# Kernel optimization log

Measured on AMD Instinct MI355X. Metric: run time of the kernel, lower is better.

Reference implementation:

```python
import jax, jax.numpy as jnp
import numpy as np

IMG = 64
N = IMG * IMG          # 4096, spatial tokens = LayerNorm dim
F2 = 128 * 128         # 16384, feature_size**2 = Mlp input dim
B, C = 8, 512
EPS = 1e-5
LOG_MAX = float(np.log(1.0 / 0.01))  # clamp max for logit_scale


def setup_inputs() -> dict:
    key = jax.random.key(0)
    ks = jax.random.split(key, 8)
    s1 = 1.0 / np.sqrt(F2)
    s2 = 1.0 / np.sqrt(N)
    return {
        "x": jax.random.normal(ks[0], (B, C, N), jnp.float32),
        "feature": jax.random.normal(ks[1], (B, C, F2), jnp.float32),
        "fc1_w": jax.random.uniform(ks[2], (N, F2), jnp.float32, -s1, s1),
        "fc1_b": jax.random.uniform(ks[3], (N,), jnp.float32, -s1, s1),
        "fc2_w": jax.random.uniform(ks[4], (N, N), jnp.float32, -s2, s2),
        "fc2_b": jax.random.uniform(ks[5], (N,), jnp.float32, -s2, s2),
        "logit_scale": jnp.full((1, 1, N), np.log(10.0), jnp.float32),
        "norm_w": jnp.ones((N,), jnp.float32),
        "norm_b": jnp.zeros((N,), jnp.float32),
    }


def reference(x, feature, fc1_w, fc1_b, fc2_w, fc2_b, logit_scale, norm_w, norm_b):
    # Mlp: (B,C,F2) -> (B,C,N), ReLU activation, drop=0
    h = jax.nn.relu(jnp.einsum('bcf,nf->bcn', feature, fc1_w) + fc1_b)
    feat = jnp.einsum('bch,nh->bcn', h, fc2_w) + fc2_b        # (B,C,N)
    feat = jnp.swapaxes(feat, 1, 2)                            # (B,N,C)
    scale = jnp.exp(jnp.minimum(logit_scale, LOG_MAX))         # (1,1,N)
    temp = jnp.einsum('bnc,bcm->bnm', feat, x) * scale         # (B,N,N)
    temp = jax.nn.softmax(temp, axis=1)                        # softmax over dim=1
    out = jnp.einsum('bcn,bnm->bcm', x, temp)                  # (B,C,N)
    # LayerNorm over last dim
    mu = jnp.mean(out, axis=-1, keepdims=True)
    var = jnp.var(out, axis=-1, keepdims=True)
    out = (out - mu) * jax.lax.rsqrt(var + EPS) * norm_w + norm_b
    return out
```

## Files before the change

### kernel.cpp

```cpp
#include <hip/hip_runtime.h>
#include <stdint.h>

using u16 = unsigned short;
typedef unsigned int u32;
typedef __attribute__((ext_vector_type(4))) float f32x4;
typedef __attribute__((ext_vector_type(8))) short short8;

typedef const __attribute__((address_space(1))) u32* gas_ptr;
typedef __attribute__((address_space(3))) u32* las_ptr;

__device__ __forceinline__ u16 f2bf_u(float f) {
    u32 u = __builtin_bit_cast(u32, f);
    u32 r = 0x7fffu + ((u >> 16) & 1u);
    return (u16)((u + r) >> 16);
}
__device__ __forceinline__ float bfu2f(u16 h) {
    u32 u = ((u32)h) << 16;
    return __builtin_bit_cast(float, u);
}
__device__ __forceinline__ void split2(float v, u16& hi, u16& lo) {
    hi = f2bf_u(v);
    lo = f2bf_u(v - bfu2f(hi));
}

__device__ __forceinline__ void gload16(const void* g, void* l) {
    __builtin_amdgcn_global_load_lds((gas_ptr)g, (las_ptr)l, 16, 0, 0);
}


#define STAGE(CBUF, KT)                                                      \
  {                                                                          \
    const int kk_ = (KT) << 5;                                               \
    _Pragma("unroll")                                                        \
    for (int it_ = 0; it_ < 2; ++it_) {                                      \
      const int rb_ = it_ * 128 + w * 16;                                    \
      const int lo_ = (CBUF) * 8192 + rb_ * 32;                              \
      const size_t ga_ = (size_t)(brow + rb_ + srow) * lda + (kk_ + sca);    \
      const size_t gb_ = (size_t)(bcol + rb_ + srow) * lda + (kk_ + sca);    \
      gload16(A0 + ga_, &As0[lo_]);                                          \
      gload16(B0 + gb_, &Bs0[lo_]);                                          \
      if constexpr (SPLIT) gload16(A1 + ga_, &As1[lo_]);                     \
    }                                                                        \
  }

#define BLOQ(Q, KT)                                                          \
  {                                                                          \
    const u16* bb_ = B1 + (size_t)(bcol + wc * 64 + lr) * lda                \
                     + (((KT) << 5) + ((l >> 4) * 8));                       \
    _Pragma("unroll")                                                        \
    for (int n_ = 0; n_ < 4; ++n_)                                           \
      Q[n_] = *(const short8*)(bb_ + (size_t)(n_ * 16) * lda);               \
  }

#define PHASE(KT, CBUF, Q)                                                   \
  {                                                                          \
    if ((KT) == NT - 1) {                                                    \
      asm volatile("s_waitcnt vmcnt(0)" ::: "memory");                       \
    } else {                                                                 \
      if constexpr (SPLIT) asm volatile("s_waitcnt vmcnt(10)" ::: "memory"); \
      else asm volatile("s_waitcnt vmcnt(4)" ::: "memory");                  \
    }                                                                        \
    __builtin_amdgcn_s_barrier();                                            \
    __builtin_amdgcn_sched_barrier(0);                                       \
    {                                                                        \
      int cs_ = (CBUF) + 2; if (cs_ >= 3) cs_ -= 3;                          \
      if ((KT) + 2 < NT) STAGE(cs_, (KT) + 2);                               \
    }                                                                        \
    short8 bh_[4];                                                           \
    _Pragma("unroll")                                                        \
    for (int n_ = 0; n_ < 4; ++n_)                                           \
      bh_[n_] = *(const short8*)&Bs0[(CBUF) * 8192 +                         \
                                     (wc * 64 + n_ * 16 + lr) * 32 + cr];    \
    _Pragma("unroll")                                                        \
    for (int mh_ = 0; mh_ < 2; ++mh_) {                                      \
      short8 ah_[4], al_[4];                                                 \
      _Pragma("unroll")                                                      \
      for (int m_ = 0; m_ < 4; ++m_) {                                       \
        const int ro_ = (CBUF) * 8192 +                                      \
                        (wr * 128 + mh_ * 64 + m_ * 16 + lr) * 32 + cr;      \
        ah_[m_] = *(const short8*)&As0[ro_];                                 \
        if constexpr (SPLIT) al_[m_] = *(const short8*)&As1[ro_];            \
      }                                                                      \
      __builtin_amdgcn_s_setprio(1);                                         \
      _Pragma("unroll")                                                      \
      for (int m_ = 0; m_ < 4; ++m_)                                         \
        _Pragma("unroll")                                                    \
        for (int n_ = 0; n_ < 4; ++n_)                                       \
          acc[mh_ * 4 + m_][n_] = __builtin_amdgcn_mfma_f32_16x16x32_bf16(   \
              ah_[m_], bh_[n_], acc[mh_ * 4 + m_][n_], 0, 0, 0);             \
      if constexpr (SPLIT) {                                                 \
        _Pragma("unroll")                                                    \
        for (int m_ = 0; m_ < 4; ++m_)                                       \
          _Pragma("unroll")                                                  \
          for (int n_ = 0; n_ < 4; ++n_)                                     \
            acc[mh_ * 4 + m_][n_] = __builtin_amdgcn_mfma_f32_16x16x32_bf16( \
                al_[m_], bh_[n_], acc[mh_ * 4 + m_][n_], 0, 0, 0);           \
        _Pragma("unroll")                                                    \
        for (int m_ = 0; m_ < 4; ++m_)                                       \
          _Pragma("unroll")                                                  \
          for (int n_ = 0; n_ < 4; ++n_)                                     \
            acc[mh_ * 4 + m_][n_] = __builtin_amdgcn_mfma_f32_16x16x32_bf16( \
                ah_[m_], Q[n_], acc[mh_ * 4 + m_][n_], 0, 0, 0);             \
      }                                                                      \
      __builtin_amdgcn_s_setprio(0);                                         \
    }                                                                        \
    __builtin_amdgcn_sched_barrier(0);                                       \
    if ((KT) + 2 < NT) {                                                     \
      if constexpr (SPLIT) BLOQ(Q, (KT) + 2);                                \
    }                                                                        \
    __builtin_amdgcn_sched_barrier(0);                                       \
  }

template<int EPI, bool SPLIT>
__global__ __launch_bounds__(512, 2)
void gemm256(const u16* __restrict__ Ah, const u16* __restrict__ Al,
             const u16* __restrict__ Bh, const u16* __restrict__ Bl,
             int K, int lda, int N,
             const float* __restrict__ aux,
             void* __restrict__ out0, void* __restrict__ out1,
             size_t strideA, size_t strideB, size_t strideO)
{
    extern __shared__ __align__(16) u16 lds[];
    u16* const As0 = lds;
    u16* const Bs0 = lds + 3 * 8192;
    u16* const As1 = SPLIT ? (lds + 6 * 8192) : lds;

    const int t = threadIdx.x;
    const int w = t >> 6;
    const int l = t & 63;

    int brow, bcol;
    const int gx = gridDim.x, gy = gridDim.y;
    const int orig = blockIdx.y * gx + blockIdx.x;
    if (gx == 16 && gy == 16) {
        const int x = orig & 7, j = orig >> 3;
        brow = ((x & 3) * 4 + (j & 3)) * 256;
        bcol = ((x >> 2) * 8 + (j >> 2)) * 256;
    } else {
        const int nwg = gx * gy;
        const int swz = (orig & 7) * (nwg >> 3) + (orig >> 3);
        brow = (swz / gx) * 256;
        bcol = (swz % gx) * 256;
    }
    const int z = blockIdx.z;

    const u16* A0 = Ah + (size_t)z * strideA;
    const u16* A1 = SPLIT ? (Al + (size_t)z * strideA) : nullptr;
    const u16* B0 = Bh + (size_t)z * strideB;
    const u16* B1 = SPLIT ? (Bl + (size_t)z * strideB) : nullptr;

    const int srow = l >> 2;
    const int sca = ((l & 3) ^ ((l >> 3) & 3)) * 8;

    const int wr = w >> 2;
    const int wc = w & 3;
    const int lr = l & 15;
    const int cr = ((l >> 4) ^ ((l >> 1) & 3)) * 8;

    f32x4 acc[8][4];
    const f32x4 zero = {0.f, 0.f, 0.f, 0.f};
#pragma unroll
    for (int i = 0; i < 8; ++i)
#pragma unroll
        for (int j = 0; j < 4; ++j) acc[i][j] = zero;

    const int NT = K >> 5;
    short8 qA[4], qB[4];

    STAGE(0, 0);
    if constexpr (SPLIT) BLOQ(qA, 0);
    STAGE(1, 1);
    if constexpr (SPLIT) BLOQ(qB, 1);

    int c = 0;
    for (int kt = 0; kt < NT; kt += 2) {
        PHASE(kt, c, qA);
        c = (c == 2) ? 0 : c + 1;
        PHASE(kt + 1, c, qB);
        c = (c == 2) ? 0 : c + 1;
    }

#pragma unroll
    for (int mh = 0; mh < 2; ++mh)
#pragma unroll
        for (int m = 0; m < 4; ++m)
#pragma unroll
            for (int n = 0; n < 4; ++n)
#pragma unroll
                for (int j = 0; j < 4; ++j) {
                    const int row = brow + wr * 128 + mh * 64 + m * 16 + (l >> 4) * 4 + j;
                    const int col = bcol + wc * 64 + n * 16 + (l & 15);
                    float v = acc[mh * 4 + m][n][j];
                    if (EPI == 0) {
                        v += aux[col];
                        v = fmaxf(v, 0.f);
                        u16 hi, lo; split2(v, hi, lo);
                        ((u16*)out0)[(size_t)row * N + col] = hi;
                        ((u16*)out1)[(size_t)row * N + col] = lo;
                    } else if (EPI == 1) {
                        v += aux[col];
                        const int bb = row >> 9, cc = row & 511;
                        const size_t idx = ((size_t)bb * N + col) * 512 + cc;
                        u16 hi, lo; split2(v, hi, lo);
                        ((u16*)out0)[idx] = hi;
                        ((u16*)out1)[idx] = lo;
                    } else if (EPI == 2) {
                        ((float*)out0)[(size_t)row * N + col] = v;
                    } else {
                        ((float*)out0)[(size_t)z * strideO + (size_t)row * N + col] = v;
                    }
                }
}

__global__ void split_k(const float* __restrict__ in, u16* __restrict__ hi,
                        u16* __restrict__ lo, size_t n4)
{
    size_t i = blockIdx.x * (size_t)blockDim.x + threadIdx.x;
    const size_t stride = (size_t)gridDim.x * blockDim.x;
    for (; i < n4; i += stride) {
        const float4 v = ((const float4*)in)[i];
        ushort4 h, l;
        split2(v.x, h.x, l.x);
        split2(v.y, h.y, l.y);
        split2(v.z, h.z, l.z);
        split2(v.w, h.w, l.w);
        ((ushort4*)hi)[i] = h;
        ((ushort4*)lo)[i] = l;
    }
}

__global__ void conv_bf16_k(const float* __restrict__ in, u16* __restrict__ out, size_t n4)
{
    size_t i = blockIdx.x * (size_t)blockDim.x + threadIdx.x;
    const size_t stride = (size_t)gridDim.x * blockDim.x;
    for (; i < n4; i += stride) {
        const float4 v = ((const float4*)in)[i];
        ushort4 o;
        o.x = f2bf_u(v.x); o.y = f2bf_u(v.y); o.z = f2bf_u(v.z); o.w = f2bf_u(v.w);
        ((ushort4*)out)[i] = o;
    }
}

__global__ void transpose_split_x(const float* __restrict__ x,
                                  u16* __restrict__ xt_hi, u16* __restrict__ xt_lo)
{
    __shared__ float tile[32][33];
    const int b = blockIdx.z;
    const int n0 = blockIdx.x * 32;
    const int c0 = blockIdx.y * 32;
    const int tx = threadIdx.x, ty = threadIdx.y;
#pragma unroll
    for (int k = 0; k < 4; ++k)
        tile[ty + 8 * k][tx] = x[((size_t)b * 512 + c0 + ty + 8 * k) * 4096 + n0 + tx];
    __syncthreads();
#pragma unroll
    for (int k = 0; k < 4; ++k) {
        const float v = tile[tx][ty + 8 * k];
        u16 hi, lo; split2(v, hi, lo);
        const size_t idx = ((size_t)b * 4096 + n0 + ty + 8 * k) * 512 + c0 + tx;
        xt_hi[idx] = hi;
        xt_lo[idx] = lo;
    }
}

__global__ void scale_prep(const float* __restrict__ ls, float* __restrict__ s)
{
    const int i = blockIdx.x * blockDim.x + threadIdx.x;
    if (i < 4096) s[i] = expf(fminf(ls[i], 4.605170185988092f));
}

__global__ __launch_bounds__(256)
void softmax_rows(const float* __restrict__ T, const float* __restrict__ s, u16* __restrict__ P)
{
    const int m = blockIdx.x;
    const int t = threadIdx.x;
    const float sc = s[m];
    const float* row = T + (size_t)m * 4096;
    float v[16];
    float mx = -3.402823e38f;
#pragma unroll
    for (int i = 0; i < 16; ++i) {
        v[i] = row[t + 256 * i] * sc;
        mx = fmaxf(mx, v[i]);
    }
#pragma unroll
    for (int o = 32; o; o >>= 1) mx = fmaxf(mx, __shfl_xor(mx, o, 64));
    __shared__ float sm[4], ss[4];
    if ((t & 63) == 0) sm[t >> 6] = mx;
    __syncthreads();
    mx = fmaxf(fmaxf(sm[0], sm[1]), fmaxf(sm[2], sm[3]));
    float sum = 0.f;
#pragma unroll
    for (int i = 0; i < 16; ++i) {
        v[i] = expf(v[i] - mx);
        sum += v[i];
    }
#pragma unroll
    for (int o = 32; o; o >>= 1) sum += __shfl_xor(sum, o, 64);
    if ((t & 63) == 0) ss[t >> 6] = sum;
    __syncthreads();
    sum = (ss[0] + ss[1]) + (ss[2] + ss[3]);
    const float inv = 1.f / sum;
#pragma unroll
    for (int i = 0; i < 16; ++i)
        P[(size_t)m * 4096 + t + 256 * i] = f2bf_u(v[i] * inv);
}

__global__ __launch_bounds__(256)
void ln_rows(const float* __restrict__ X, const float* __restrict__ gw,
             const float* __restrict__ gb, float* __restrict__ out)
{
    const int r = blockIdx.x;
    const int t = threadIdx.x;
    const float* row = X + (size_t)r * 4096;
    float v[16];
    float s1 = 0.f, s2 = 0.f;
#pragma unroll
    for (int i = 0; i < 16; ++i) {
        v[i] = row[t + 256 * i];
        s1 += v[i];
        s2 += v[i] * v[i];
    }
#pragma unroll
    for (int o = 32; o; o >>= 1) {
        s1 += __shfl_xor(s1, o, 64);
        s2 += __shfl_xor(s2, o, 64);
    }
    __shared__ float m1[4], m2[4];
    if ((t & 63) == 0) { m1[t >> 6] = s1; m2[t >> 6] = s2; }
    __syncthreads();
    s1 = (m1[0] + m1[1]) + (m1[2] + m1[3]);
    s2 = (m2[0] + m2[1]) + (m2[2] + m2[3]);
    const float mu = s1 * (1.f / 4096.f);
    const float var = s2 * (1.f / 4096.f) - mu * mu;
    const float rs = rsqrtf(var + 1e-5f);
#pragma unroll
    for (int i = 0; i < 16; ++i) {
        const int n = t + 256 * i;
        out[(size_t)r * 4096 + n] = (v[i] - mu) * rs * gw[n] + gb[n];
    }
}

extern "C" void kernel_launch(void* const* d_in, const int* in_sizes, int n_in,
                              void* d_out, int out_size, void* d_ws, size_t ws_size,
                              hipStream_t stream)
{
    const float* x  = (const float*)d_in[0];
    const float* fe = (const float*)d_in[1];
    const float* w1 = (const float*)d_in[2];
    const float* b1 = (const float*)d_in[3];
    const float* w2 = (const float*)d_in[4];
    const float* b2 = (const float*)d_in[5];
    const float* ls = (const float*)d_in[6];
    const float* nw = (const float*)d_in[7];
    const float* nb = (const float*)d_in[8];
    float* out = (float*)d_out;
    char* ws = (char*)d_ws;

    if (ws_size < 637550592ull) return;

    hipFuncSetAttribute((const void*)gemm256<0, true>,
                        hipFuncAttributeMaxDynamicSharedMemorySize, 147456);
    hipFuncSetAttribute((const void*)gemm256<1, true>,
                        hipFuncAttributeMaxDynamicSharedMemorySize, 147456);
    hipFuncSetAttribute((const void*)gemm256<2, true>,
                        hipFuncAttributeMaxDynamicSharedMemorySize, 147456);
    hipFuncSetAttribute((const void*)gemm256<3, false>,
                        hipFuncAttributeMaxDynamicSharedMemorySize, 98304);

    u16*  fhi  = (u16*) (ws + 0ull);
    u16*  flo  = (u16*) (ws + 134217728ull);
    u16*  w1hi = (u16*) (ws + 268435456ull);
    u16*  w1lo = (u16*) (ws + 402653184ull);
    u16*  hhi  = (u16*) (ws + 536870912ull);
    u16*  hlo  = (u16*) (ws + 570425344ull);
    u16*  w2hi = (u16*) (ws + 0ull);
    u16*  w2lo = (u16*) (ws + 33554432ull);
    u16*  fthi = (u16*) (ws + 67108864ull);
    u16*  ftlo = (u16*) (ws + 100663296ull);
    u16*  xthi = (u16*) (ws + 134217728ull);
    u16*  xtlo = (u16*) (ws + 167772160ull);
    u16*  xbf  = (u16*) (ws + 201326592ull);
    float* tt  = (float*)(ws + 234881024ull);
    u16*  pall = (u16*) (ws + 301989888ull);
    float* pre = (float*)(ws + 570425344ull);
    float* sv  = (float*)(ws + 637534208ull);

    split_k<<<2048, 256, 0, stream>>>(fe, fhi, flo, (size_t)16777216);
    split_k<<<2048, 256, 0, stream>>>(w1, w1hi, w1lo, (size_t)16777216);

    gemm256<0, true><<<dim3(16, 16, 1), 512, 147456, stream>>>(
        fhi, flo, w1hi, w1lo, 16384, 16384, 4096, b1, hhi, hlo, 0, 0, 0);

    split_k<<<2048, 256, 0, stream>>>(w2, w2hi, w2lo, (size_t)4194304);

    gemm256<1, true><<<dim3(16, 16, 1), 512, 147456, stream>>>(
        hhi, hlo, w2hi, w2lo, 4096, 4096, 4096, b2, fthi, ftlo, 0, 0, 0);

    transpose_split_x<<<dim3(128, 16, 8), dim3(32, 8), 0, stream>>>(x, xthi, xtlo);
    conv_bf16_k<<<2048, 256, 0, stream>>>(x, xbf, (size_t)4194304);
    scale_prep<<<16, 256, 0, stream>>>(ls, sv);

    for (int b = 0; b < 8; ++b) {
        const size_t o = (size_t)b * 4096 * 512;
        gemm256<2, true><<<dim3(16, 16, 1), 512, 147456, stream>>>(
            xthi + o, xtlo + o, fthi + o, ftlo + o, 512, 512, 4096,
            nullptr, tt, nullptr, 0, 0, 0);
        softmax_rows<<<4096, 256, 0, stream>>>(tt, sv, pall + (size_t)b * 16777216);
    }

    gemm256<3, false><<<dim3(16, 2, 8), 512, 98304, stream>>>(
        xbf, nullptr, pall, nullptr, 4096, 4096, 4096, nullptr, pre, nullptr,
        (size_t)512 * 4096, (size_t)4096 * 4096, (size_t)512 * 4096);

    ln_rows<<<4096, 256, 0, stream>>>(pre, nw, nb, out);
}
```

Baseline: 2.691 ms.

## Restructure GEMM k-loop to issue prefetch first and wait after MFMAs

Rewrites the per-k-tile phase so the next stage's global-to-LDS loads and the register prefetch of the low B split are issued at the start of the tile. All A fragments are read from LDS up front, and the MFMA groups run before the vmcnt wait and the workgroup barrier. The waitcnt and barrier move from the top of each tile to its end, with an initial wait added before the loop. The aim is to hide global-load latency behind the MFMA work and to reduce stalls at the barrier. In exchange, more A fragments are live in registers at once, which raises register pressure, and the vmcnt counts must stay correct for the reordered loads.

```diff
diff --git a/kernel.cpp b/kernel.cpp
--- a/kernel.cpp
+++ b/kernel.cpp
@@ -52,62 +52,89 @@
       Q[n_] = *(const short8*)(bb_ + (size_t)(n_ * 16) * lda);               \
   }
 
-#define PHASE(KT, CBUF, Q)                                                   \
+#define TILE(KT, CB, QCUR, QNXT)                                             \
   {                                                                          \
-    if ((KT) == NT - 1) {                                                    \
-      asm volatile("s_waitcnt vmcnt(0)" ::: "memory");                       \
-    } else {                                                                 \
-      if constexpr (SPLIT) asm volatile("s_waitcnt vmcnt(10)" ::: "memory"); \
-      else asm volatile("s_waitcnt vmcnt(4)" ::: "memory");                  \
-    }                                                                        \
-    __builtin_amdgcn_s_barrier();                                            \
+                      \
+    if ((KT) + 2 < NT) {                                                     \
+      int cs_ = (CB) + 2; if (cs_ >= 3) cs_ -= 3;                            \
+      STAGE(cs_, (KT) + 2);                                                  \
+    }                                                                        \
+    if constexpr (SPLIT) { if ((KT) + 1 < NT) BLOQ(QNXT, (KT) + 1); }        \
     __builtin_amdgcn_sched_barrier(0);                                       \
-    {                                                                        \
-      int cs_ = (CBUF) + 2; if (cs_ >= 3) cs_ -= 3;                          \
-      if ((KT) + 2 < NT) STAGE(cs_, (KT) + 2);                               \
-    }                                                                        \
-    short8 bh_[4];                                                           \
+                                        \
+    short8 bh_[4], ah0_[4], ah1_[4], al0_[4], al1_[4];                       \
     _Pragma("unroll")                                                        \
     for (int n_ = 0; n_ < 4; ++n_)                                           \
-      bh_[n_] = *(const short8*)&Bs0[(CBUF) * 8192 +                         \
+      bh_[n_] = *(const short8*)&Bs0[(CB) * 8192 +                           \
                                      (wc * 64 + n_ * 16 + lr) * 32 + cr];    \
     _Pragma("unroll")                                                        \
-    for (int mh_ = 0; mh_ < 2; ++mh_) {                                      \
-      short8 ah_[4], al_[4];                                                 \
+    for (int m_ = 0; m_ < 4; ++m_) {                                         \
+      const int r0_ = (CB) * 8192 + (wr * 128 + m_ * 16 + lr) * 32 + cr;     \
+      ah0_[m_] = *(const short8*)&As0[r0_];                                  \
+      ah1_[m_] = *(const short8*)&As0[r0_ + 64 * 32];                        \
+      if constexpr (SPLIT) {                                                 \
+        al0_[m_] = *(const short8*)&As1[r0_];                                \
+        al1_[m_] = *(const short8*)&As1[r0_ + 64 * 32];                      \
+      }                                                                      \
+    }                                                                        \
+    __builtin_amdgcn_sched_barrier(0);                                       \
+                                               \
+    __builtin_amdgcn_s_setprio(1);                                           \
+    _Pragma("unroll")                                                        \
+    for (int m_ = 0; m_ < 4; ++m_)                                           \
       _Pragma("unroll")                                                      \
-      for (int m_ = 0; m_ < 4; ++m_) {                                       \
-        const int ro_ = (CBUF) * 8192 +                                      \
-                        (wr * 128 + mh_ * 64 + m_ * 16 + lr) * 32 + cr;      \
-        ah_[m_] = *(const short8*)&As0[ro_];                                 \
-        if constexpr (SPLIT) al_[m_] = *(const short8*)&As1[ro_];            \
+      for (int n_ = 0; n_ < 4; ++n_) {                                       \
+        acc[m_][n_] = __builtin_amdgcn_mfma_f32_16x16x32_bf16(               \
+            ah0_[m_], bh_[n_], acc[m_][n_], 0, 0, 0);                        \
+        acc[4 + m_][n_] = __builtin_amdgcn_mfma_f32_16x16x32_bf16(           \
+            ah1_[m_], bh_[n_], acc[4 + m_][n_], 0, 0, 0);                    \
       }                                                                      \
+    __builtin_amdgcn_s_setprio(0);                                           \
+    __builtin_amdgcn_sched_barrier(0);                                       \
+    if constexpr (SPLIT) {                                                   \
+                                                \
       __builtin_amdgcn_s_setprio(1);                                         \
       _Pragma("unroll")                                                      \
       for (int m_ = 0; m_ < 4; ++m_)                                         \
         _Pragma("unroll")                                                    \
-        for (int n_ = 0; n_ < 4; ++n_)                                       \
-          acc[mh_ * 4 + m_][n_] = __builtin_amdgcn_mfma_f32_16x16x32_bf16(   \
-              ah_[m_], bh_[n_], acc[mh_ * 4 + m_][n_], 0, 0, 0);             \
-      if constexpr (SPLIT) {                                                 \
+        for (int n_ = 0; n_ < 4; ++n_) {                                     \
+          acc[m_][n_] = __builtin_amdgcn_mfma_f32_16x16x32_bf16(             \
+              al0_[m_], bh_[n_], acc[m_][n_], 0, 0, 0);                      \
+          acc[4 + m_][n_] = __builtin_amdgcn_mfma_f32_16x16x32_bf16(         \
+              al1_[m_], bh_[n_], acc[4 + m_][n_], 0, 0, 0);                  \
+        }                                                                    \
+      __builtin_amdgcn_s_setprio(0);                                         \
+      __builtin_amdgcn_sched_barrier(0);                                     \
+    }                                                                        \
+                   \
+    if ((KT) + 2 < NT) {                                                     \
+      if constexpr (SPLIT)                                                   \
+        asm volatile("s_waitcnt vmcnt(10)" ::: "memory");                    \
+      else                                                                   \
+        asm volatile("s_waitcnt vmcnt(4)" ::: "memory");                     \
+    } else if ((KT) + 1 < NT) {                                              \
+      if constexpr (SPLIT)                                                   \
+        asm volatile("s_waitcnt vmcnt(4)" ::: "memory");                     \
+      else                                                                   \
+        asm volatile("s_waitcnt vmcnt(0)" ::: "memory");                     \
+    } else {                                                                 \
+      asm volatile("s_waitcnt vmcnt(0)" ::: "memory");                       \
+    }                                                                        \
+    __builtin_amdgcn_sched_barrier(0);                                       \
+    if constexpr (SPLIT) {                                                   \
+      __builtin_amdgcn_s_setprio(1);                                         \
+      _Pragma("unroll")                                                      \
+      for (int m_ = 0; m_ < 4; ++m_)                                         \
         _Pragma("unroll")                                                    \
-        for (int m_ = 0; m_ < 4; ++m_)                                       \
-          _Pragma("unroll")                                                  \
-          for (int n_ = 0; n_ < 4; ++n_)                                     \
-            acc[mh_ * 4 + m_][n_] = __builtin_amdgcn_mfma_f32_16x16x32_bf16( \
-                al_[m_], bh_[n_], acc[mh_ * 4 + m_][n_], 0, 0, 0);           \
-        _Pragma("unroll")                                                    \
-        for (int m_ = 0; m_ < 4; ++m_)                                       \
-          _Pragma("unroll")                                                  \
-          for (int n_ = 0; n_ < 4; ++n_)                                     \
-            acc[mh_ * 4 + m_][n_] = __builtin_amdgcn_mfma_f32_16x16x32_bf16( \
-                ah_[m_], Q[n_], acc[mh_ * 4 + m_][n_], 0, 0, 0);             \
-      }                                                                      \
+        for (int n_ = 0; n_ < 4; ++n_) {                                     \
+          acc[m_][n_] = __builtin_amdgcn_mfma_f32_16x16x32_bf16(             \
+              ah0_[m_], QCUR[n_], acc[m_][n_], 0, 0, 0);                     \
+          acc[4 + m_][n_] = __builtin_amdgcn_mfma_f32_16x16x32_bf16(         \
+              ah1_[m_], QCUR[n_], acc[4 + m_][n_], 0, 0, 0);                 \
+        }                                                                    \
       __builtin_amdgcn_s_setprio(0);                                         \
     }                                                                        \
-    __builtin_amdgcn_sched_barrier(0);                                       \
-    if ((KT) + 2 < NT) {                                                     \
-      if constexpr (SPLIT) BLOQ(Q, (KT) + 2);                                \
-    }                                                                        \
+    __builtin_amdgcn_s_barrier();                                            \
     __builtin_amdgcn_sched_barrier(0);                                       \
   }
 
@@ -170,14 +197,19 @@
     STAGE(0, 0);
     if constexpr (SPLIT) BLOQ(qA, 0);
     STAGE(1, 1);
-    if constexpr (SPLIT) BLOQ(qB, 1);
-
-    int c = 0;
+    if constexpr (SPLIT)
+        asm volatile("s_waitcnt vmcnt(10)" ::: "memory");
+    else
+        asm volatile("s_waitcnt vmcnt(4)" ::: "memory");
+    __builtin_amdgcn_s_barrier();
+    __builtin_amdgcn_sched_barrier(0);
+
+    int cb = 0;
     for (int kt = 0; kt < NT; kt += 2) {
-        PHASE(kt, c, qA);
-        c = (c == 2) ? 0 : c + 1;
-        PHASE(kt + 1, c, qB);
-        c = (c == 2) ? 0 : c + 1;
+        TILE(kt, cb, qA, qB);
+        cb = (cb == 2) ? 0 : cb + 1;
+        TILE(kt + 1, cb, qB, qA);
+        cb = (cb == 2) ? 0 : cb + 1;
     }
 
 #pragma unroll
```

New measurement: 7.118 ms. 2.65x slower.

## Switch GEMM inner loop from 16x16x32 to 32x32x16 bf16 MFMA tiles

Applied to the files above, without the earlier changes.

Replaces the 16x16x32 MFMA tiling with 32x32x16 MFMA instructions. Each warp now holds 4x2 accumulator tiles of 16 floats, and the LDS fragment loads, direct global B-low loads and epilogue index mapping are adjusted to match. The larger instruction needs fewer LDS fragment reads per FLOP and fewer MFMA issues. A prologue wait and barrier are also added before the main loop. This risks different register pressure and LDS bank patterns, and the swizzle mapping has to stay consistent with the staged layout.

```diff
diff --git a/kernel.cpp b/kernel.cpp
--- a/kernel.cpp
+++ b/kernel.cpp
@@ -3,7 +3,7 @@
 
 using u16 = unsigned short;
 typedef unsigned int u32;
-typedef __attribute__((ext_vector_type(4))) float f32x4;
+typedef __attribute__((ext_vector_type(16))) float f32x16;
 typedef __attribute__((ext_vector_type(8))) short short8;
 
 typedef const __attribute__((address_space(1))) u32* gas_ptr;
@@ -45,14 +45,15 @@
 
 #define BLOQ(Q, KT)                                                          \
   {                                                                          \
-    const u16* bb_ = B1 + (size_t)(bcol + wc * 64 + lr) * lda                \
-                     + (((KT) << 5) + ((l >> 4) * 8));                       \
-    _Pragma("unroll")                                                        \
-    for (int n_ = 0; n_ < 4; ++n_)                                           \
-      Q[n_] = *(const short8*)(bb_ + (size_t)(n_ * 16) * lda);               \
+    const u16* bb_ = B1 + (size_t)(bcol + wc * 64 + l31) * lda               \
+                     + (((KT) << 5) + hi5 * 8);                              \
+    Q[0] = *(const short8*)(bb_);                                \
+    Q[1] = *(const short8*)(bb_ + 16);                           \
+    Q[2] = *(const short8*)(bb_ + (size_t)32 * lda);             \
+    Q[3] = *(const short8*)(bb_ + (size_t)32 * lda + 16);        \
   }
 
-#define PHASE(KT, CBUF, Q)                                                   \
+#define PHASE(KT, CB, Q)                                                     \
   {                                                                          \
     if ((KT) == NT - 1) {                                                    \
       asm volatile("s_waitcnt vmcnt(0)" ::: "memory");                       \
@@ -63,51 +64,47 @@
     __builtin_amdgcn_s_barrier();                                            \
     __builtin_amdgcn_sched_barrier(0);                                       \
     {                                                                        \
-      int cs_ = (CBUF) + 2; if (cs_ >= 3) cs_ -= 3;                          \
+      int cs_ = (CB) + 2; if (cs_ >= 3) cs_ -= 3;                            \
       if ((KT) + 2 < NT) STAGE(cs_, (KT) + 2);                               \
     }                                                                        \
-    short8 bh_[4];                                                           \
+    short8 bh_[2][2];                                                        \
     _Pragma("unroll")                                                        \
-    for (int n_ = 0; n_ < 4; ++n_)                                           \
-      bh_[n_] = *(const short8*)&Bs0[(CBUF) * 8192 +                         \
-                                     (wc * 64 + n_ * 16 + lr) * 32 + cr];    \
+    for (int cg_ = 0; cg_ < 2; ++cg_)                                        \
+      _Pragma("unroll")                                                      \
+      for (int s_ = 0; s_ < 2; ++s_)                                         \
+        bh_[cg_][s_] = *(const short8*)&Bs0[(CB) * 8192 +                    \
+            (wc * 64 + cg_ * 32 + l31) * 32 + crs[s_]];                      \
     _Pragma("unroll")                                                        \
-    for (int mh_ = 0; mh_ < 2; ++mh_) {                                      \
-      short8 ah_[4], al_[4];                                                 \
+    for (int rg_ = 0; rg_ < 4; ++rg_) {                                      \
+      short8 ah_[2], al_[2];                                                 \
+      const int ro_ = (CB) * 8192 + (wr * 128 + rg_ * 32 + l31) * 32;        \
       _Pragma("unroll")                                                      \
-      for (int m_ = 0; m_ < 4; ++m_) {                                       \
-        const int ro_ = (CBUF) * 8192 +                                      \
-                        (wr * 128 + mh_ * 64 + m_ * 16 + lr) * 32 + cr;      \
-        ah_[m_] = *(const short8*)&As0[ro_];                                 \
-        if constexpr (SPLIT) al_[m_] = *(const short8*)&As1[ro_];            \
+      for (int s_ = 0; s_ < 2; ++s_) {                                       \
+        ah_[s_] = *(const short8*)&As0[ro_ + crs[s_]];                       \
+        if constexpr (SPLIT) al_[s_] = *(const short8*)&As1[ro_ + crs[s_]];  \
       }                                                                      \
       __builtin_amdgcn_s_setprio(1);                                         \
       _Pragma("unroll")                                                      \
-      for (int m_ = 0; m_ < 4; ++m_)                                         \
+      for (int s_ = 0; s_ < 2; ++s_) {                                       \
         _Pragma("unroll")                                                    \
-        for (int n_ = 0; n_ < 4; ++n_)                                       \
-          acc[mh_ * 4 + m_][n_] = __builtin_amdgcn_mfma_f32_16x16x32_bf16(   \
-              ah_[m_], bh_[n_], acc[mh_ * 4 + m_][n_], 0, 0, 0);             \
-      if constexpr (SPLIT) {                                                 \
-        _Pragma("unroll")                                                    \
-        for (int m_ = 0; m_ < 4; ++m_)                                       \
+        for (int cg_ = 0; cg_ < 2; ++cg_)                                    \
+          acc[rg_][cg_] = __builtin_amdgcn_mfma_f32_32x32x16_bf16(           \
+              ah_[s_], bh_[cg_][s_], acc[rg_][cg_], 0, 0, 0);                \
+        if constexpr (SPLIT) {                                               \
           _Pragma("unroll")                                                  \
-          for (int n_ = 0; n_ < 4; ++n_)                                     \
-            acc[mh_ * 4 + m_][n_] = __builtin_amdgcn_mfma_f32_16x16x32_bf16( \
-                al_[m_], bh_[n_], acc[mh_ * 4 + m_][n_], 0, 0, 0);           \
-        _Pragma("unroll")                                                    \
-        for (int m_ = 0; m_ < 4; ++m_)                                       \
+          for (int cg_ = 0; cg_ < 2; ++cg_)                                  \
+            acc[rg_][cg_] = __builtin_amdgcn_mfma_f32_32x32x16_bf16(         \
+                al_[s_], bh_[cg_][s_], acc[rg_][cg_], 0, 0, 0);              \
           _Pragma("unroll")                                                  \
-          for (int n_ = 0; n_ < 4; ++n_)                                     \
-            acc[mh_ * 4 + m_][n_] = __builtin_amdgcn_mfma_f32_16x16x32_bf16( \
-                ah_[m_], Q[n_], acc[mh_ * 4 + m_][n_], 0, 0, 0);             \
+          for (int cg_ = 0; cg_ < 2; ++cg_)                                  \
+            acc[rg_][cg_] = __builtin_amdgcn_mfma_f32_32x32x16_bf16(         \
+                ah_[s_], Q[cg_ * 2 + s_], acc[rg_][cg_], 0, 0, 0);           \
+        }                                                                    \
       }                                                                      \
       __builtin_amdgcn_s_setprio(0);                                         \
     }                                                                        \
     __builtin_amdgcn_sched_barrier(0);                                       \
-    if ((KT) + 2 < NT) {                                                     \
-      if constexpr (SPLIT) BLOQ(Q, (KT) + 2);                                \
-    }                                                                        \
+    if ((KT) + 2 < NT) { if constexpr (SPLIT) BLOQ(Q, (KT) + 2); }           \
     __builtin_amdgcn_sched_barrier(0);                                       \
   }
 
@@ -154,15 +151,20 @@
 
     const int wr = w >> 2;
     const int wc = w & 3;
-    const int lr = l & 15;
-    const int cr = ((l >> 4) ^ ((l >> 1) & 3)) * 8;
-
-    f32x4 acc[8][4];
-    const f32x4 zero = {0.f, 0.f, 0.f, 0.f};
-#pragma unroll
-    for (int i = 0; i < 8; ++i)
-#pragma unroll
-        for (int j = 0; j < 4; ++j) acc[i][j] = zero;
+    const int l31 = l & 31;
+    const int hi5 = l >> 5;
+    const int csw = (l >> 1) & 3;
+    int crs[2];
+    crs[0] = ((hi5) ^ csw) * 8;
+    crs[1] = ((2 + hi5) ^ csw) * 8;
+
+    f32x16 acc[4][2];
+#pragma unroll
+    for (int i = 0; i < 4; ++i)
+#pragma unroll
+        for (int j = 0; j < 2; ++j)
+#pragma unroll
+            for (int r = 0; r < 16; ++r) acc[i][j][r] = 0.f;
 
     const int NT = K >> 5;
     short8 qA[4], qB[4];
@@ -171,45 +173,49 @@
     if constexpr (SPLIT) BLOQ(qA, 0);
     STAGE(1, 1);
     if constexpr (SPLIT) BLOQ(qB, 1);
-
-    int c = 0;
+    if constexpr (SPLIT)
+        asm volatile("s_waitcnt vmcnt(10)" ::: "memory");
+    else
+        asm volatile("s_waitcnt vmcnt(4)" ::: "memory");
+    __builtin_amdgcn_s_barrier();
+    __builtin_amdgcn_sched_barrier(0);
+
+    int cb = 0;
     for (int kt = 0; kt < NT; kt += 2) {
-        PHASE(kt, c, qA);
-        c = (c == 2) ? 0 : c + 1;
-        PHASE(kt + 1, c, qB);
-        c = (c == 2) ? 0 : c + 1;
-    }
-
-#pragma unroll
-    for (int mh = 0; mh < 2; ++mh)
-#pragma unroll
-        for (int m = 0; m < 4; ++m)
-#pragma unroll
-            for (int n = 0; n < 4; ++n)
-#pragma unroll
-                for (int j = 0; j < 4; ++j) {
-                    const int row = brow + wr * 128 + mh * 64 + m * 16 + (l >> 4) * 4 + j;
-                    const int col = bcol + wc * 64 + n * 16 + (l & 15);
-                    float v = acc[mh * 4 + m][n][j];
-                    if (EPI == 0) {
-                        v += aux[col];
-                        v = fmaxf(v, 0.f);
-                        u16 hi, lo; split2(v, hi, lo);
-                        ((u16*)out0)[(size_t)row * N + col] = hi;
-                        ((u16*)out1)[(size_t)row * N + col] = lo;
-                    } else if (EPI == 1) {
-                        v += aux[col];
-                        const int bb = row >> 9, cc = row & 511;
-                        const size_t idx = ((size_t)bb * N + col) * 512 + cc;
-                        u16 hi, lo; split2(v, hi, lo);
-                        ((u16*)out0)[idx] = hi;
-                        ((u16*)out1)[idx] = lo;
-                    } else if (EPI == 2) {
-                        ((float*)out0)[(size_t)row * N + col] = v;
-                    } else {
-                        ((float*)out0)[(size_t)z * strideO + (size_t)row * N + col] = v;
-                    }
+        PHASE(kt, cb, qA);
+        cb = (cb == 2) ? 0 : cb + 1;
+        PHASE(kt + 1, cb, qB);
+        cb = (cb == 2) ? 0 : cb + 1;
+    }
+
+#pragma unroll
+    for (int rg = 0; rg < 4; ++rg)
+#pragma unroll
+        for (int cg = 0; cg < 2; ++cg)
+#pragma unroll
+            for (int r = 0; r < 16; ++r) {
+                const int row = brow + wr * 128 + rg * 32 + (r & 3) + 8 * (r >> 2) + 4 * hi5;
+                const int col = bcol + wc * 64 + cg * 32 + l31;
+                float v = acc[rg][cg][r];
+                if (EPI == 0) {
+                    v += aux[col];
+                    v = fmaxf(v, 0.f);
+                    u16 hi, lo; split2(v, hi, lo);
+                    ((u16*)out0)[(size_t)row * N + col] = hi;
+                    ((u16*)out1)[(size_t)row * N + col] = lo;
+                } else if (EPI == 1) {
+                    v += aux[col];
+                    const int bb = row >> 9, cc = row & 511;
+                    const size_t idx = ((size_t)bb * N + col) * 512 + cc;
+                    u16 hi, lo; split2(v, hi, lo);
+                    ((u16*)out0)[idx] = hi;
+                    ((u16*)out1)[idx] = lo;
+                } else if (EPI == 2) {
+                    ((float*)out0)[(size_t)row * N + col] = v;
+                } else {
+                    ((float*)out0)[(size_t)z * strideO + (size_t)row * N + col] = v;
                 }
+            }
 }
 
 __global__ void split_k(const float* __restrict__ in, u16* __restrict__ hi,
```

New measurement: 2.953 ms. 9.8% more time.

## Replace 256x256 triple-buffered GEMM with 128x128 double-buffered kernel

Applied to the files above, without the earlier changes.

The GEMM kernel shrinks from 256x256 output tiles with 8 waves and a three-stage LDS ring to 128x128 tiles with 4 waves and a two-stage buffer synchronised by __syncthreads. The hand-tuned vmcnt waits, sched barriers and the special 16x16 grid swizzle are dropped in favour of a generic swizzle, and grids grow accordingly. Smaller tiles need less LDS and allow more resident blocks, but they lower arithmetic intensity, raise global and L2 traffic for these large bf16x3 GEMMs, and give up the deeper prefetch.

```diff
diff --git a/kernel.cpp b/kernel.cpp
--- a/kernel.cpp
+++ b/kernel.cpp
@@ -26,6 +26,8 @@
 __device__ __forceinline__ void gload16(const void* g, void* l) {
     __builtin_amdgcn_global_load_lds((gas_ptr)g, (las_ptr)l, 16, 0, 0);
 }
+
+#define MFMA16(A, B, C) __builtin_amdgcn_mfma_f32_16x16x32_bf16((A), (B), (C), 0, 0, 0)
 
 
 #define STAGE(CBUF, KT)                                                      \
@@ -33,8 +35,8 @@
     const int kk_ = (KT) << 5;                                               \
     _Pragma("unroll")                                                        \
     for (int it_ = 0; it_ < 2; ++it_) {                                      \
-      const int rb_ = it_ * 128 + w * 16;                                    \
-      const int lo_ = (CBUF) * 8192 + rb_ * 32;                              \
+      const int rb_ = it_ * 64 + w * 16;                                     \
+      const int lo_ = (CBUF) * 4096 + rb_ * 32;                              \
       const size_t ga_ = (size_t)(brow + rb_ + srow) * lda + (kk_ + sca);    \
       const size_t gb_ = (size_t)(bcol + rb_ + srow) * lda + (kk_ + sca);    \
       gload16(A0 + ga_, &As0[lo_]);                                          \
@@ -52,68 +54,43 @@
       Q[n_] = *(const short8*)(bb_ + (size_t)(n_ * 16) * lda);               \
   }
 
-#define PHASE(KT, CBUF, Q)                                                   \
+#define TILE(KT, CUR, QC, QN)                                                \
   {                                                                          \
-    if ((KT) == NT - 1) {                                                    \
-      asm volatile("s_waitcnt vmcnt(0)" ::: "memory");                       \
-    } else {                                                                 \
-      if constexpr (SPLIT) asm volatile("s_waitcnt vmcnt(10)" ::: "memory"); \
-      else asm volatile("s_waitcnt vmcnt(4)" ::: "memory");                  \
-    }                                                                        \
-    __builtin_amdgcn_s_barrier();                                            \
-    __builtin_amdgcn_sched_barrier(0);                                       \
-    {                                                                        \
-      int cs_ = (CBUF) + 2; if (cs_ >= 3) cs_ -= 3;                          \
-      if ((KT) + 2 < NT) STAGE(cs_, (KT) + 2);                               \
+    if ((KT) + 1 < NT) {                                                     \
+      STAGE((CUR) ^ 1, (KT) + 1);                                            \
+      if constexpr (SPLIT) BLOQ(QN, (KT) + 1);                               \
     }                                                                        \
     short8 bh_[4];                                                           \
     _Pragma("unroll")                                                        \
     for (int n_ = 0; n_ < 4; ++n_)                                           \
-      bh_[n_] = *(const short8*)&Bs0[(CBUF) * 8192 +                         \
+      bh_[n_] = *(const short8*)&Bs0[(CUR) * 4096 +                          \
                                      (wc * 64 + n_ * 16 + lr) * 32 + cr];    \
     _Pragma("unroll")                                                        \
-    for (int mh_ = 0; mh_ < 2; ++mh_) {                                      \
-      short8 ah_[4], al_[4];                                                 \
-      _Pragma("unroll")                                                      \
-      for (int m_ = 0; m_ < 4; ++m_) {                                       \
-        const int ro_ = (CBUF) * 8192 +                                      \
-                        (wr * 128 + mh_ * 64 + m_ * 16 + lr) * 32 + cr;      \
-        ah_[m_] = *(const short8*)&As0[ro_];                                 \
-        if constexpr (SPLIT) al_[m_] = *(const short8*)&As1[ro_];            \
-      }                                                                      \
+    for (int m_ = 0; m_ < 4; ++m_) {                                         \
+      const int ro_ = (CUR) * 4096 + (lrw + m_ * 16) * 32 + cr;              \
+      short8 ah_ = *(const short8*)&As0[ro_];                                \
+      short8 al_;                                                            \
+      if constexpr (SPLIT) al_ = *(const short8*)&As1[ro_];                  \
       __builtin_amdgcn_s_setprio(1);                                         \
       _Pragma("unroll")                                                      \
-      for (int m_ = 0; m_ < 4; ++m_)                                         \
+      for (int n_ = 0; n_ < 4; ++n_)                                         \
+        acc[m_][n_] = MFMA16(ah_, bh_[n_], acc[m_][n_]);                     \
+      if constexpr (SPLIT) {                                                 \
         _Pragma("unroll")                                                    \
         for (int n_ = 0; n_ < 4; ++n_)                                       \
-          acc[mh_ * 4 + m_][n_] = __builtin_amdgcn_mfma_f32_16x16x32_bf16(   \
-              ah_[m_], bh_[n_], acc[mh_ * 4 + m_][n_], 0, 0, 0);             \
-      if constexpr (SPLIT) {                                                 \
+          acc[m_][n_] = MFMA16(al_, bh_[n_], acc[m_][n_]);                   \
         _Pragma("unroll")                                                    \
-        for (int m_ = 0; m_ < 4; ++m_)                                       \
-          _Pragma("unroll")                                                  \
-          for (int n_ = 0; n_ < 4; ++n_)                                     \
-            acc[mh_ * 4 + m_][n_] = __builtin_amdgcn_mfma_f32_16x16x32_bf16( \
-                al_[m_], bh_[n_], acc[mh_ * 4 + m_][n_], 0, 0, 0);           \
-        _Pragma("unroll")                                                    \
-        for (int m_ = 0; m_ < 4; ++m_)                                       \
-          _Pragma("unroll")                                                  \
-          for (int n_ = 0; n_ < 4; ++n_)                                     \
-            acc[mh_ * 4 + m_][n_] = __builtin_amdgcn_mfma_f32_16x16x32_bf16( \
-                ah_[m_], Q[n_], acc[mh_ * 4 + m_][n_], 0, 0, 0);             \
+        for (int n_ = 0; n_ < 4; ++n_)                                       \
+          acc[m_][n_] = MFMA16(ah_, QC[n_], acc[m_][n_]);                    \
       }                                                                      \
       __builtin_amdgcn_s_setprio(0);                                         \
     }                                                                        \
-    __builtin_amdgcn_sched_barrier(0);                                       \
-    if ((KT) + 2 < NT) {                                                     \
-      if constexpr (SPLIT) BLOQ(Q, (KT) + 2);                                \
-    }                                                                        \
-    __builtin_amdgcn_sched_barrier(0);                                       \
+    __syncthreads();                                                         \
   }
 
 template<int EPI, bool SPLIT>
-__global__ __launch_bounds__(512, 2)
-void gemm256(const u16* __restrict__ Ah, const u16* __restrict__ Al,
+__global__ __launch_bounds__(256, 3)
+void gemm128(const u16* __restrict__ Ah, const u16* __restrict__ Al,
              const u16* __restrict__ Bh, const u16* __restrict__ Bl,
              int K, int lda, int N,
              const float* __restrict__ aux,
@@ -122,26 +99,19 @@
 {
     extern __shared__ __align__(16) u16 lds[];
     u16* const As0 = lds;
-    u16* const Bs0 = lds + 3 * 8192;
-    u16* const As1 = SPLIT ? (lds + 6 * 8192) : lds;
+    u16* const Bs0 = lds + 2 * 4096;
+    u16* const As1 = SPLIT ? (lds + 4 * 4096) : lds;
 
     const int t = threadIdx.x;
     const int w = t >> 6;
     const int l = t & 63;
 
-    int brow, bcol;
-    const int gx = gridDim.x, gy = gridDim.y;
+    const int gx = gridDim.x;
+    const int nwg = gx * gridDim.y;
     const int orig = blockIdx.y * gx + blockIdx.x;
-    if (gx == 16 && gy == 16) {
-        const int x = orig & 7, j = orig >> 3;
-        brow = ((x & 3) * 4 + (j & 3)) * 256;
-        bcol = ((x >> 2) * 8 + (j >> 2)) * 256;
-    } else {
-        const int nwg = gx * gy;
-        const int swz = (orig & 7) * (nwg >> 3) + (orig >> 3);
-        brow = (swz / gx) * 256;
-        bcol = (swz % gx) * 256;
-    }
+    const int swz = (orig & 7) * (nwg >> 3) + (orig >> 3);
+    const int brow = (swz / gx) * 128;
+    const int bcol = (swz % gx) * 128;
     const int z = blockIdx.z;
 
     const u16* A0 = Ah + (size_t)z * strideA;
@@ -152,15 +122,16 @@
     const int srow = l >> 2;
     const int sca = ((l & 3) ^ ((l >> 3) & 3)) * 8;
 
-    const int wr = w >> 2;
-    const int wc = w & 3;
+    const int wr = w >> 1;
+    const int wc = w & 1;
     const int lr = l & 15;
     const int cr = ((l >> 4) ^ ((l >> 1) & 3)) * 8;
-
-    f32x4 acc[8][4];
+    const int lrw = wr * 64 + lr;
+
+    f32x4 acc[4][4];
     const f32x4 zero = {0.f, 0.f, 0.f, 0.f};
 #pragma unroll
-    for (int i = 0; i < 8; ++i)
+    for (int i = 0; i < 4; ++i)
 #pragma unroll
         for (int j = 0; j < 4; ++j) acc[i][j] = zero;
 
@@ -169,47 +140,41 @@
 
     STAGE(0, 0);
     if constexpr (SPLIT) BLOQ(qA, 0);
-    STAGE(1, 1);
-    if constexpr (SPLIT) BLOQ(qB, 1);
-
-    int c = 0;
+    __syncthreads();
+
     for (int kt = 0; kt < NT; kt += 2) {
-        PHASE(kt, c, qA);
-        c = (c == 2) ? 0 : c + 1;
-        PHASE(kt + 1, c, qB);
-        c = (c == 2) ? 0 : c + 1;
-    }
-
-#pragma unroll
-    for (int mh = 0; mh < 2; ++mh)
-#pragma unroll
-        for (int m = 0; m < 4; ++m)
-#pragma unroll
-            for (int n = 0; n < 4; ++n)
-#pragma unroll
-                for (int j = 0; j < 4; ++j) {
-                    const int row = brow + wr * 128 + mh * 64 + m * 16 + (l >> 4) * 4 + j;
-                    const int col = bcol + wc * 64 + n * 16 + (l & 15);
-                    float v = acc[mh * 4 + m][n][j];
-                    if (EPI == 0) {
-                        v += aux[col];
-                        v = fmaxf(v, 0.f);
-                        u16 hi, lo; split2(v, hi, lo);
-                        ((u16*)out0)[(size_t)row * N + col] = hi;
-                        ((u16*)out1)[(size_t)row * N + col] = lo;
-                    } else if (EPI == 1) {
-                        v += aux[col];
-                        const int bb = row >> 9, cc = row & 511;
-                        const size_t idx = ((size_t)bb * N + col) * 512 + cc;
-                        u16 hi, lo; split2(v, hi, lo);
-                        ((u16*)out0)[idx] = hi;
-                        ((u16*)out1)[idx] = lo;
-                    } else if (EPI == 2) {
-                        ((float*)out0)[(size_t)row * N + col] = v;
-                    } else {
-                        ((float*)out0)[(size_t)z * strideO + (size_t)row * N + col] = v;
-                    }
+        TILE(kt, 0, qA, qB);
+        TILE(kt + 1, 1, qB, qA);
+    }
+
+#pragma unroll
+    for (int m = 0; m < 4; ++m)
+#pragma unroll
+        for (int n = 0; n < 4; ++n)
+#pragma unroll
+            for (int j = 0; j < 4; ++j) {
+                const int row = brow + wr * 64 + m * 16 + (l >> 4) * 4 + j;
+                const int col = bcol + wc * 64 + n * 16 + (l & 15);
+                float v = acc[m][n][j];
+                if (EPI == 0) {
+                    v += aux[col];
+                    v = fmaxf(v, 0.f);
+                    u16 hi, lo; split2(v, hi, lo);
+                    ((u16*)out0)[(size_t)row * N + col] = hi;
+                    ((u16*)out1)[(size_t)row * N + col] = lo;
+                } else if (EPI == 1) {
+                    v += aux[col];
+                    const int bb = row >> 9, cc = row & 511;
+                    const size_t idx = ((size_t)bb * N + col) * 512 + cc;
+                    u16 hi, lo; split2(v, hi, lo);
+                    ((u16*)out0)[idx] = hi;
+                    ((u16*)out1)[idx] = lo;
+                } else if (EPI == 2) {
+                    ((float*)out0)[(size_t)row * N + col] = v;
+                } else {
+                    ((float*)out0)[(size_t)z * strideO + (size_t)row * N + col] = v;
                 }
+            }
 }
 
 __global__ void split_k(const float* __restrict__ in, u16* __restrict__ hi,
@@ -359,14 +324,14 @@
 
     if (ws_size < 637550592ull) return;
 
-    hipFuncSetAttribute((const void*)gemm256<0, true>,
-                        hipFuncAttributeMaxDynamicSharedMemorySize, 147456);
-    hipFuncSetAttribute((const void*)gemm256<1, true>,
-                        hipFuncAttributeMaxDynamicSharedMemorySize, 147456);
-    hipFuncSetAttribute((const void*)gemm256<2, true>,
-                        hipFuncAttributeMaxDynamicSharedMemorySize, 147456);
-    hipFuncSetAttribute((const void*)gemm256<3, false>,
-                        hipFuncAttributeMaxDynamicSharedMemorySize, 98304);
+    hipFuncSetAttribute((const void*)gemm128<0, true>,
+                        hipFuncAttributeMaxDynamicSharedMemorySize, 49152);
+    hipFuncSetAttribute((const void*)gemm128<1, true>,
+                        hipFuncAttributeMaxDynamicSharedMemorySize, 49152);
+    hipFuncSetAttribute((const void*)gemm128<2, true>,
+                        hipFuncAttributeMaxDynamicSharedMemorySize, 49152);
+    hipFuncSetAttribute((const void*)gemm128<3, false>,
+                        hipFuncAttributeMaxDynamicSharedMemorySize, 32768);
 
     u16*  fhi  = (u16*) (ws + 0ull);
     u16*  flo  = (u16*) (ws + 134217728ull);
@@ -389,12 +354,12 @@
     split_k<<<2048, 256, 0, stream>>>(fe, fhi, flo, (size_t)16777216);
     split_k<<<2048, 256, 0, stream>>>(w1, w1hi, w1lo, (size_t)16777216);
 
-    gemm256<0, true><<<dim3(16, 16, 1), 512, 147456, stream>>>(
+    gemm128<0, true><<<dim3(32, 32, 1), 256, 49152, stream>>>(
         fhi, flo, w1hi, w1lo, 16384, 16384, 4096, b1, hhi, hlo, 0, 0, 0);
 
     split_k<<<2048, 256, 0, stream>>>(w2, w2hi, w2lo, (size_t)4194304);
 
-    gemm256<1, true><<<dim3(16, 16, 1), 512, 147456, stream>>>(
+    gemm128<1, true><<<dim3(32, 32, 1), 256, 49152, stream>>>(
         hhi, hlo, w2hi, w2lo, 4096, 4096, 4096, b2, fthi, ftlo, 0, 0, 0);
 
     transpose_split_x<<<dim3(128, 16, 8), dim3(32, 8), 0, stream>>>(x, xthi, xtlo);
@@ -403,13 +368,13 @@
 
     for (int b = 0; b < 8; ++b) {
         const size_t o = (size_t)b * 4096 * 512;
-        gemm256<2, true><<<dim3(16, 16, 1), 512, 147456, stream>>>(
+        gemm128<2, true><<<dim3(32, 32, 1), 256, 49152, stream>>>(
             xthi + o, xtlo + o, fthi + o, ftlo + o, 512, 512, 4096,
             nullptr, tt, nullptr, 0, 0, 0);
         softmax_rows<<<4096, 256, 0, stream>>>(tt, sv, pall + (size_t)b * 16777216);
     }
 
-    gemm256<3, false><<<dim3(16, 2, 8), 512, 98304, stream>>>(
+    gemm128<3, false><<<dim3(32, 4, 8), 256, 32768, stream>>>(
         xbf, nullptr, pall, nullptr, 4096, 4096, 4096, nullptr, pre, nullptr,
         (size_t)512 * 4096, (size_t)4096 * 4096, (size_t)512 * 4096);
 
```

Result: slower. 4.242 ms (+57.6%).
